# Kernel optimization log

Measured on AMD Instinct MI355X. Metric: run time of the kernel, lower is better.

Reference implementation:

```python
import jax, jax.numpy as jnp
import numpy as np

R, N, E = 3, 50000, 800000
IN, HID, HEADS, OUT = 128, 64, 2, 64


def setup_inputs() -> dict:
    key = jax.random.key(0)
    ks = jax.random.split(key, 12)
    s = 0.05
    return {
        "x": jax.random.normal(ks[0], (N, IN), jnp.float32),
        "src": jax.random.randint(ks[1], (R, E), 0, N, jnp.int32),
        "dst": jax.random.randint(ks[2], (R, E), 0, N, jnp.int32),
        "W1": jax.random.normal(ks[3], (R, IN, HEADS * HID), jnp.float32) * s,
        "al1": jax.random.normal(ks[4], (R, HEADS, HID), jnp.float32) * s,
        "ar1": jax.random.normal(ks[5], (R, HEADS, HID), jnp.float32) * s,
        "b1": jnp.zeros((R, HEADS * HID), jnp.float32),
        "W2": jax.random.normal(ks[6], (R, HEADS * HID, HID), jnp.float32) * s,
        "al2": jax.random.normal(ks[7], (R, 1, HID), jnp.float32) * s,
        "ar2": jax.random.normal(ks[8], (R, 1, HID), jnp.float32) * s,
        "b2": jnp.zeros((R, HID), jnp.float32),
        "Wl": jax.random.normal(ks[9], (HID, OUT), jnp.float32) * s,
        "bl": jnp.zeros((OUT,), jnp.float32),
    }


def gat_conv(x, src, dst, W, al, ar, b, heads, dim):
    """DGL GATConv on a homogeneous edge list: returns elu(aggregated) [N, heads, dim]."""
    n = x.shape[0]
    feat = (x @ W).reshape(n, heads, dim)                     # [N,H,D]
    el = (feat * al).sum(-1)                                  # [N,H]
    er = (feat * ar).sum(-1)                                  # [N,H]
    e = jax.nn.leaky_relu(el[src] + er[dst], 0.2)             # [E,H]
    # segment softmax over incoming edges of each dst node
    m = jax.lax.stop_gradient(jax.ops.segment_max(e, dst, num_segments=n))
    ee = jnp.exp(e - m[dst])                                  # [E,H]
    z = jax.ops.segment_sum(ee, dst, num_segments=n)          # [N,H]
    a = ee / z[dst]                                           # [E,H]
    msg = feat[src] * a[..., None]                            # [E,H,D]
    out = jax.ops.segment_sum(msg, dst, num_segments=n)       # [N,H,D]
    return jax.nn.elu(out + b.reshape(1, heads, dim))


def reference(x, src, dst, W1, al1, ar1, b1, W2, al2, ar2, b2, Wl, bl):
    # layer 1: per-relation GATConv, summed (HeteroGraphConv default aggregate='sum')
    h1 = sum(gat_conv(x, src[r], dst[r], W1[r], al1[r], ar1[r], b1[r], HEADS, HID)
             for r in range(R))                               # [N,H,HID]
    h1 = h1.reshape(N, HEADS * HID)                           # flatten(1)
    # layer 2: single-head GATConv per relation, summed
    h2 = sum(gat_conv(h1, src[r], dst[r], W2[r], al2[r], ar2[r], b2[r], 1, HID)
             for r in range(R))                               # [N,1,HID]
    h2 = h2.mean(1)                                           # mean over the single head
    return h2 @ Wl + bl                                       # [N,OUT]
```

## Files before the change

kernel.cpp:

```cpp
#include <hip/hip_runtime.h>

constexpr int R = 3;
constexpr int N = 50000;
constexpr int E = 800000;
constexpr int K = 128;
constexpr int NT16 = N / 16;
constexpr int GB = (NT16 + 3) / 4;

constexpr int BKT_SH = 9;
constexpr int NBKT = (N + 511) >> 9;
constexpr int BCAP = 10240;
constexpr int P1E = 4096;
constexpr int P1B = (E + P1E - 1) / P1E;

constexpr int NF1 = 192;
constexpr int NF2 = 96;
constexpr int NF3 = 16;

typedef __attribute__((ext_vector_type(8))) short bf16x8;
typedef __attribute__((ext_vector_type(4))) float f32x4;
typedef __attribute__((ext_vector_type(2))) float f32x2;


__device__ inline unsigned short f2bf(float f) {
    unsigned u = __float_as_uint(f);
    u += 0x7FFF + ((u >> 16) & 1);
    return (unsigned short)(u >> 16);
}
__device__ inline float bf2f_lo(unsigned p) { return __uint_as_float(p << 16); }
__device__ inline float bf2f_hi(unsigned p) { return __uint_as_float(p & 0xFFFF0000u); }

__device__ inline float lrelu02(float x) { return fmaxf(x, 0.2f * x); }
__device__ inline float elu1f(float x) { return x > 0.f ? x : __expf(x) - 1.f; }


__global__ __launch_bounds__(256) void bucket_p1(const int* __restrict__ src,
                                                 const int* __restrict__ dst,
                                                 int* __restrict__ gcur,
                                                 uint2* __restrict__ ebuf) {
    __shared__ uint2 img[P1E];
    __shared__ int bins[NBKT], bstart[NBKT], gbase[NBKT];
    __shared__ int sc[128];
    const int r = blockIdx.y;
    const int e0 = blockIdx.x * P1E;
    const int cnt = min(P1E, E - e0);
    const int tid = threadIdx.x;
    if (tid < NBKT) bins[tid] = 0;
    __syncthreads();
    int sv[16], dv[16], rk[16];
    int ni = 0;
    for (int i = tid; i < cnt; i += 256, ni++) {
        sv[ni] = src[(size_t)r * E + e0 + i];
        dv[ni] = dst[(size_t)r * E + e0 + i];
        rk[ni] = atomicAdd(&bins[dv[ni] >> BKT_SH], 1);
    }
    __syncthreads();
    if (tid < 128) sc[tid] = (tid < NBKT) ? bins[tid] : 0;
    __syncthreads();
    for (int off = 1; off < 128; off <<= 1) {
        int v = 0;
        if (tid < 128 && tid >= off) v = sc[tid - off];
        __syncthreads();
        if (tid < 128) sc[tid] += v;
        __syncthreads();
    }
    if (tid < NBKT) bstart[tid] = sc[tid] - bins[tid];
    __syncthreads();
    for (int j = 0; j < ni; j++) {
        int b = dv[j] >> BKT_SH;
        img[bstart[b] + rk[j]] = make_uint2((unsigned)sv[j], (unsigned)dv[j]);
    }
    if (tid < NBKT) gbase[tid] = bins[tid] ? atomicAdd(&gcur[r * NBKT + tid], bins[tid]) : 0;
    __syncthreads();
    for (int i = tid; i < cnt; i += 256) {
        uint2 e = img[i];
        int b = (int)(e.y >> BKT_SH);
        int pos = gbase[b] + (i - bstart[b]);
        if (pos < BCAP) ebuf[(size_t)(r * NBKT + b) * BCAP + pos] = e;
    }
}

__global__ void bucket_scan(const int* __restrict__ gcur, int* __restrict__ bpre) {
    int w = threadIdx.x >> 6, lane = threadIdx.x & 63;
    if (w >= R) return;
    const int* g = gcur + w * NBKT;
    int* p = bpre + w * NBKT;
    int carry = 0;
    for (int base = 0; base < NBKT; base += 64) {
        int v = (base + lane < NBKT) ? g[base + lane] : 0;
        int x = v;
#pragma unroll
        for (int off = 1; off < 64; off <<= 1) {
            int t = __shfl_up(x, off);
            if (lane >= off) x += t;
        }
        if (base + lane < NBKT) p[base + lane] = carry + x - v;
        carry += __shfl(x, 63);
    }
}

__global__ __launch_bounds__(256) void bucket_p2(const uint2* __restrict__ ebuf,
                                                 const int* __restrict__ gcur,
                                                 const int* __restrict__ bpre,
                                                 int* __restrict__ rowptr,
                                                 int* __restrict__ srclist) {
    __shared__ unsigned img[BCAP];
    __shared__ int bins[512], bst[512], cur[512], sc[256];
    const int r = blockIdx.y, b = blockIdx.x;
    const int tid = threadIdx.x;
    const int bcnt = gcur[r * NBKT + b];
    const int gbase = bpre[r * NBKT + b];
    const uint2* reg = ebuf + (size_t)(r * NBKT + b) * BCAP;
    for (int i = tid; i < 512; i += 256) bins[i] = 0;
    __syncthreads();
    for (int i = tid; i < bcnt; i += 256) atomicAdd(&bins[reg[i].y & 511], 1);
    __syncthreads();
    int v0 = bins[2 * tid], v1 = bins[2 * tid + 1];
    sc[tid] = v0 + v1;
    __syncthreads();
    for (int off = 1; off < 256; off <<= 1) {
        int t = 0;
        if (tid >= off) t = sc[tid - off];
        __syncthreads();
        sc[tid] += t;
        __syncthreads();
    }
    int base = sc[tid] - (v0 + v1);
    bst[2 * tid] = base;
    bst[2 * tid + 1] = base + v0;
    cur[2 * tid] = base;
    cur[2 * tid + 1] = base + v0;
    __syncthreads();
    for (int nl = tid; nl < 512; nl += 256) {
        int n = (b << BKT_SH) + nl;
        if (n < N) rowptr[r * (N + 1) + n] = gbase + bst[nl];
    }
    if (b == NBKT - 1 && tid == 0) rowptr[r * (N + 1) + N] = gbase + bcnt;
    for (int i = tid; i < bcnt; i += 256) {
        uint2 e = reg[i];
        int p = atomicAdd(&cur[e.y & 511], 1);
        img[p] = e.x;
    }
    __syncthreads();
    for (int i = tid; i < bcnt; i += 256) srclist[(size_t)r * E + gbase + i] = img[i];
}


__global__ __launch_bounds__(64) void prep_wf(const float* __restrict__ W1,
                                              const float* __restrict__ W2,
                                              const float* __restrict__ Wl,
                                              short* __restrict__ WF1,
                                              short* __restrict__ WF2,
                                              short* __restrict__ WF3) {
    int f = blockIdx.x;
    int lane = threadIdx.x;
    int c = lane & 15, g = lane >> 4;
    const float* srcp;
    int stride;
    short* dstp;
    int hl;
    if (f < NF1) {
        hl = f & 1;
        int h = (f >> 1) & 1, ks = (f >> 2) & 3, tr = (f >> 4) & 3, r = f >> 6;
        int col = h * 64 + tr * 16 + c;
        srcp = W1 + (size_t)r * 128 * 128 + (size_t)(ks * 32 + g * 8) * 128 + col;
        stride = 128;
        dstp = WF1 + (size_t)f * 512 + lane * 8;
    } else if (f < NF1 + NF2) {
        int f2 = f - NF1;
        hl = f2 & 1;
        int ks = (f2 >> 1) & 3, t = f2 >> 3;
        int c192 = t * 16 + c;
        int r = c192 >> 6, col64 = c192 & 63;
        srcp = W2 + (size_t)r * 128 * 64 + (size_t)(ks * 32 + g * 8) * 64 + col64;
        stride = 64;
        dstp = WF2 + (size_t)f2 * 512 + lane * 8;
    } else {
        int f3 = f - NF1 - NF2;
        hl = f3 & 1;
        int ks = (f3 >> 1) & 1, t = f3 >> 2;
        srcp = Wl + (size_t)(ks * 32 + g * 8) * 64 + t * 16 + c;
        stride = 64;
        dstp = WF3 + (size_t)f3 * 512 + lane * 8;
    }
#pragma unroll
    for (int i = 0; i < 8; i++) {
        float v = srcp[(size_t)i * stride];
        unsigned short hi = f2bf(v);
        dstp[i] = hl ? (short)f2bf(v - __uint_as_float(((unsigned)hi) << 16)) : (short)hi;
    }
}


__device__ inline void split_a_p(const float* __restrict__ xrow, bf16x8* ah, bf16x8* al) {
#pragma unroll
    for (int ks = 0; ks < 4; ks++) {
        f32x4 xa = *(const f32x4*)(xrow + ks * 32);
        f32x4 xb = *(const f32x4*)(xrow + ks * 32 + 4);
#pragma unroll
        for (int i = 0; i < 4; i++) {
            unsigned short h = f2bf(xa[i]);
            ah[ks][i] = (short)h;
            al[ks][i] = (short)f2bf(xa[i] - __uint_as_float(((unsigned)h) << 16));
            unsigned short h2 = f2bf(xb[i]);
            ah[ks][4 + i] = (short)h2;
            al[ks][4 + i] = (short)f2bf(xb[i] - __uint_as_float(((unsigned)h2) << 16));
        }
    }
}

__global__ __launch_bounds__(256) void gemm1_mfma(const float* __restrict__ X,
                                                  const short* __restrict__ WF1,
                                                  const float* __restrict__ al1,
                                                  const float* __restrict__ ar1,
                                                  unsigned* __restrict__ packed1,
                                                  float* __restrict__ el,
                                                  float* __restrict__ er) {
    __shared__ float xs[64][132];
    const int n0_blk = blockIdx.x * 64;
    const int tid = threadIdx.x;
    const int rows = min(64, N - n0_blk);
    for (int i = tid; i < rows * 32; i += 256) {
        int row = i >> 5, q4 = i & 31;
        *(f32x4*)&xs[row][q4 * 4] = *(const f32x4*)(X + (size_t)(n0_blk + row) * K + q4 * 4);
    }
    __syncthreads();
    const int lane = tid & 63;
    const int c = lane & 15;
    const int g = lane >> 4;
    const int n0 = n0_blk + (tid >> 6) * 16;
    if (n0 >= N) return;
    bf16x8 ah[4], al[4];
    split_a_p(&xs[(tid >> 6) * 16 + c][g * 8], ah, al);
    const bf16x8* fbase = (const bf16x8*)WF1 + lane;
    for (int r = 0; r < R; r++) {
        float pel0[4] = {0.f, 0.f, 0.f, 0.f}, per0[4] = {0.f, 0.f, 0.f, 0.f};
        float pel1[4] = {0.f, 0.f, 0.f, 0.f}, per1[4] = {0.f, 0.f, 0.f, 0.f};
        for (int tr = 0; tr < 4; tr++) {
            const bf16x8* fb = fbase + (size_t)((r * 4 + tr) * 16) * 64;
            f32x4 acc0 = {0.f, 0.f, 0.f, 0.f};
            f32x4 acc1 = {0.f, 0.f, 0.f, 0.f};
#pragma unroll
            for (int ks = 0; ks < 4; ks++) {
                bf16x8 b0h = fb[(ks * 4 + 0) * 64];
                bf16x8 b0l = fb[(ks * 4 + 1) * 64];
                bf16x8 b1h = fb[(ks * 4 + 2) * 64];
                bf16x8 b1l = fb[(ks * 4 + 3) * 64];
                acc0 = __builtin_amdgcn_mfma_f32_16x16x32_bf16(ah[ks], b0h, acc0, 0, 0, 0);
                acc0 = __builtin_amdgcn_mfma_f32_16x16x32_bf16(al[ks], b0h, acc0, 0, 0, 0);
                acc0 = __builtin_amdgcn_mfma_f32_16x16x32_bf16(ah[ks], b0l, acc0, 0, 0, 0);
                acc1 = __builtin_amdgcn_mfma_f32_16x16x32_bf16(ah[ks], b1h, acc1, 0, 0, 0);
                acc1 = __builtin_amdgcn_mfma_f32_16x16x32_bf16(al[ks], b1h, acc1, 0, 0, 0);
                acc1 = __builtin_amdgcn_mfma_f32_16x16x32_bf16(ah[ks], b1l, acc1, 0, 0, 0);
            }
            float a0 = al1[r * 128 + tr * 16 + c];
            float r0 = ar1[r * 128 + tr * 16 + c];
            float a1 = al1[r * 128 + 64 + tr * 16 + c];
            float r1 = ar1[r * 128 + 64 + tr * 16 + c];
#pragma unroll
            for (int i = 0; i < 4; i++) {
                pel0[i] += acc0[i] * a0;
                per0[i] += acc0[i] * r0;
                pel1[i] += acc1[i] * a1;
                per1[i] += acc1[i] * r1;
                int m = g * 4 + i;
                unsigned wrd = (unsigned)f2bf(acc0[i]) | ((unsigned)f2bf(acc1[i]) << 16);
                packed1[(size_t)(n0 + m) * 192 + r * 64 + tr * 16 + c] = wrd;
            }
        }
#pragma unroll
        for (int off = 1; off < 16; off <<= 1) {
#pragma unroll
            for (int i = 0; i < 4; i++) {
                pel0[i] += __shfl_xor(pel0[i], off);
                per0[i] += __shfl_xor(per0[i], off);
                pel1[i] += __shfl_xor(pel1[i], off);
                per1[i] += __shfl_xor(per1[i], off);
            }
        }
        if (c == 0) {
#pragma unroll
            for (int i = 0; i < 4; i++) {
                int n = n0 + g * 4 + i;
                el[(r * N + n) * 2 + 0] = pel0[i];
                el[(r * N + n) * 2 + 1] = pel1[i];
                er[(r * N + n) * 2 + 0] = per0[i];
                er[(r * N + n) * 2 + 1] = per1[i];
            }
        }
    }
}


__global__ __launch_bounds__(256) void gemm2_mfma(const float* __restrict__ X,
                                                  const short* __restrict__ WF2,
                                                  const float* __restrict__ al2,
                                                  const float* __restrict__ ar2,
                                                  unsigned short* __restrict__ packed2,
                                                  float* __restrict__ el,
                                                  float* __restrict__ er) {
    __shared__ float xs[64][132];
    const int n0_blk = blockIdx.x * 64;
    const int tid = threadIdx.x;
    const int rows = min(64, N - n0_blk);
    for (int i = tid; i < rows * 32; i += 256) {
        int row = i >> 5, q4 = i & 31;
        *(f32x4*)&xs[row][q4 * 4] = *(const f32x4*)(X + (size_t)(n0_blk + row) * K + q4 * 4);
    }
    __syncthreads();
    const int lane = tid & 63;
    const int c = lane & 15;
    const int g = lane >> 4;
    const int n0 = n0_blk + (tid >> 6) * 16;
    if (n0 >= N) return;
    bf16x8 ah[4], al[4];
    split_a_p(&xs[(tid >> 6) * 16 + c][g * 8], ah, al);
    const bf16x8* fbase = (const bf16x8*)WF2 + lane;
    float pel[4], per[4];
    for (int t = 0; t < 12; t++) {
        int r = t >> 2, tt = t & 3;
        if (tt == 0) {
#pragma unroll
            for (int i = 0; i < 4; i++) { pel[i] = 0.f; per[i] = 0.f; }
        }
        f32x4 acc = {0.f, 0.f, 0.f, 0.f};
#pragma unroll
        for (int ks = 0; ks < 4; ks++) {
            bf16x8 vh = fbase[(size_t)((t * 4 + ks) * 2 + 0) * 64];
            bf16x8 vl = fbase[(size_t)((t * 4 + ks) * 2 + 1) * 64];
            acc = __builtin_amdgcn_mfma_f32_16x16x32_bf16(ah[ks], vh, acc, 0, 0, 0);
            acc = __builtin_amdgcn_mfma_f32_16x16x32_bf16(al[ks], vh, acc, 0, 0, 0);
            acc = __builtin_amdgcn_mfma_f32_16x16x32_bf16(ah[ks], vl, acc, 0, 0, 0);
        }
        float a = al2[r * 64 + tt * 16 + c];
        float rr = ar2[r * 64 + tt * 16 + c];
#pragma unroll
        for (int i = 0; i < 4; i++) {
            pel[i] += acc[i] * a;
            per[i] += acc[i] * rr;
            int m = g * 4 + i;
            packed2[(size_t)(n0 + m) * 192 + t * 16 + c] = f2bf(acc[i]);
        }
        if (tt == 3) {
#pragma unroll
            for (int off = 1; off < 16; off <<= 1) {
#pragma unroll
                for (int i = 0; i < 4; i++) {
                    pel[i] += __shfl_xor(pel[i], off);
                    per[i] += __shfl_xor(per[i], off);
                }
            }
            if (c == 0) {
#pragma unroll
                for (int i = 0; i < 4; i++) {
                    int n = n0 + g * 4 + i;
                    el[r * N + n] = pel[i];
                    er[r * N + n] = per[i];
                }
            }
        }
    }
}


__global__ __launch_bounds__(256) void agg_l1(const char* __restrict__ packed1b,
                                              const float* __restrict__ el_,
                                              const float* __restrict__ er_,
                                              const int* __restrict__ rowptr,
                                              const int* __restrict__ srclist,
                                              const float* __restrict__ b1,
                                              float* __restrict__ h1) {
    int n = (blockIdx.x * blockDim.x + threadIdx.x) >> 6;
    int lane = threadIdx.x & 63;
    if (n >= N) return;
    const int q = lane >> 4;
    const int c = lane & 15;
    const unsigned coff = (unsigned)(c * 16);
    const float2* el2 = (const float2*)el_;
    const float2* er2 = (const float2*)er_;
    float hacc0[4] = {0.f, 0.f, 0.f, 0.f}, hacc1[4] = {0.f, 0.f, 0.f, 0.f};
    for (int r = 0; r < R; r++) {
        int beg = rowptr[r * (N + 1) + n];
        int end = rowptr[r * (N + 1) + n + 1];
        float2 ern = er2[r * N + n];
        const int* sl = srclist + r * E;
        const int rbase = r * N;
        const unsigned robf = (unsigned)(r * 256);
        f32x2 acc2[4] = {{0.f, 0.f}, {0.f, 0.f}, {0.f, 0.f}, {0.f, 0.f}};
        float zl0 = 0.f, zl1 = 0.f;
        for (int cbeg = beg; cbeg < end; cbeg += 64) {
            int cnt = min(64, end - cbeg);
            unsigned ofs = 0;
            float ew0 = 0.f, ew1 = 0.f;
            if (lane < cnt) {
                int sid = sl[cbeg + lane];
                float2 e = el2[rbase + sid];
                ew0 = __expf(lrelu02(e.x + ern.x));
                ew1 = __expf(lrelu02(e.y + ern.y));
                ofs = (unsigned)sid * 768u + robf;
            }
            zl0 += ew0;
            zl1 += ew1;
            int kmax = (cnt + 3) & ~3;
            int k = 0;
            for (; k + 8 <= kmax; k += 8) {
                int iA = k + q, iB = k + 4 + q;
                unsigned oA = (unsigned)__shfl((int)ofs, iA);
                unsigned oB = (unsigned)__shfl((int)ofs, iB);
                f32x2 wA = {__shfl(ew0, iA), __shfl(ew1, iA)};
                f32x2 wB = {__shfl(ew0, iB), __shfl(ew1, iB)};
                uint4 vA = *(const uint4*)(packed1b + (oA + coff));
                uint4 vB = *(const uint4*)(packed1b + (oB + coff));
                acc2[0] += (f32x2){bf2f_lo(vA.x), bf2f_hi(vA.x)} * wA;
                acc2[1] += (f32x2){bf2f_lo(vA.y), bf2f_hi(vA.y)} * wA;
                acc2[2] += (f32x2){bf2f_lo(vA.z), bf2f_hi(vA.z)} * wA;
                acc2[3] += (f32x2){bf2f_lo(vA.w), bf2f_hi(vA.w)} * wA;
                acc2[0] += (f32x2){bf2f_lo(vB.x), bf2f_hi(vB.x)} * wB;
                acc2[1] += (f32x2){bf2f_lo(vB.y), bf2f_hi(vB.y)} * wB;
                acc2[2] += (f32x2){bf2f_lo(vB.z), bf2f_hi(vB.z)} * wB;
                acc2[3] += (f32x2){bf2f_lo(vB.w), bf2f_hi(vB.w)} * wB;
            }
            if (k < kmax) {
                int idx = k + q;
                unsigned o = (unsigned)__shfl((int)ofs, idx);
                f32x2 w = {__shfl(ew0, idx), __shfl(ew1, idx)};
                uint4 v = *(const uint4*)(packed1b + (o + coff));
                acc2[0] += (f32x2){bf2f_lo(v.x), bf2f_hi(v.x)} * w;
                acc2[1] += (f32x2){bf2f_lo(v.y), bf2f_hi(v.y)} * w;
                acc2[2] += (f32x2){bf2f_lo(v.z), bf2f_hi(v.z)} * w;
                acc2[3] += (f32x2){bf2f_lo(v.w), bf2f_hi(v.w)} * w;
            }
        }
#pragma unroll
        for (int i = 0; i < 4; i++) {
            acc2[i].x += __shfl_xor(acc2[i].x, 16);
            acc2[i].x += __shfl_xor(acc2[i].x, 32);
            acc2[i].y += __shfl_xor(acc2[i].y, 16);
            acc2[i].y += __shfl_xor(acc2[i].y, 32);
        }
#pragma unroll
        for (int off = 32; off; off >>= 1) {
            zl0 += __shfl_xor(zl0, off);
            zl1 += __shfl_xor(zl1, off);
        }
        float rz0 = (end > beg) ? __builtin_amdgcn_rcpf(zl0) : 0.f;
        float rz1 = (end > beg) ? __builtin_amdgcn_rcpf(zl1) : 0.f;
        float4 bv0 = *(const float4*)(b1 + r * 128 + c * 4);
        float4 bv1 = *(const float4*)(b1 + r * 128 + 64 + c * 4);
        hacc0[0] += elu1f(acc2[0].x * rz0 + bv0.x);
        hacc0[1] += elu1f(acc2[1].x * rz0 + bv0.y);
        hacc0[2] += elu1f(acc2[2].x * rz0 + bv0.z);
        hacc0[3] += elu1f(acc2[3].x * rz0 + bv0.w);
        hacc1[0] += elu1f(acc2[0].y * rz1 + bv1.x);
        hacc1[1] += elu1f(acc2[1].y * rz1 + bv1.y);
        hacc1[2] += elu1f(acc2[2].y * rz1 + bv1.z);
        hacc1[3] += elu1f(acc2[3].y * rz1 + bv1.w);
    }
    if (q == 0) {
        float4 o0 = {hacc0[0], hacc0[1], hacc0[2], hacc0[3]};
        float4 o1 = {hacc1[0], hacc1[1], hacc1[2], hacc1[3]};
        *(float4*)(h1 + (size_t)n * 128 + c * 4) = o0;
        *(float4*)(h1 + (size_t)n * 128 + 64 + c * 4) = o1;
    }
}

__global__ __launch_bounds__(256) void agg_l2(const char* __restrict__ packed2b,
                                              const float* __restrict__ el,
                                              const float* __restrict__ er,
                                              const int* __restrict__ rowptr,
                                              const int* __restrict__ srclist,
                                              const float* __restrict__ b2,
                                              float* __restrict__ h2) {
    int n = (blockIdx.x * blockDim.x + threadIdx.x) >> 6;
    int lane = threadIdx.x & 63;
    if (n >= N) return;
    const int q = lane >> 4;
    const int c = lane & 15;
    const unsigned coff = (unsigned)(c * 8);
    float hacc[4] = {0.f, 0.f, 0.f, 0.f};
    for (int r = 0; r < R; r++) {
        int beg = rowptr[r * (N + 1) + n];
        int end = rowptr[r * (N + 1) + n + 1];
        float ern = er[r * N + n];
        const int* sl = srclist + r * E;
        const int rbase = r * N;
        const unsigned robf = (unsigned)(r * 128);
        f32x2 acc01 = {0.f, 0.f}, acc23 = {0.f, 0.f};
        float zl = 0.f;
        for (int cbeg = beg; cbeg < end; cbeg += 64) {
            int cnt = min(64, end - cbeg);
            unsigned ofs = 0;
            float ew = 0.f;
            if (lane < cnt) {
                int sid = sl[cbeg + lane];
                ew = __expf(lrelu02(el[rbase + sid] + ern));
                ofs = (unsigned)sid * 384u + robf;
            }
            zl += ew;
            int kmax = (cnt + 3) & ~3;
            int k = 0;
            for (; k + 8 <= kmax; k += 8) {
                int iA = k + q, iB = k + 4 + q;
                unsigned oA = (unsigned)__shfl((int)ofs, iA);
                unsigned oB = (unsigned)__shfl((int)ofs, iB);
                float aA = __shfl(ew, iA), aB = __shfl(ew, iB);
                uint2 vA = *(const uint2*)(packed2b + (oA + coff));
                uint2 vB = *(const uint2*)(packed2b + (oB + coff));
                f32x2 wA = {aA, aA}, wB = {aB, aB};
                acc01 += (f32x2){bf2f_lo(vA.x), bf2f_hi(vA.x)} * wA;
                acc23 += (f32x2){bf2f_lo(vA.y), bf2f_hi(vA.y)} * wA;
                acc01 += (f32x2){bf2f_lo(vB.x), bf2f_hi(vB.x)} * wB;
                acc23 += (f32x2){bf2f_lo(vB.y), bf2f_hi(vB.y)} * wB;
            }
            if (k < kmax) {
                int idx = k + q;
                unsigned o = (unsigned)__shfl((int)ofs, idx);
                float a = __shfl(ew, idx);
                uint2 v = *(const uint2*)(packed2b + (o + coff));
                f32x2 w = {a, a};
                acc01 += (f32x2){bf2f_lo(v.x), bf2f_hi(v.x)} * w;
                acc23 += (f32x2){bf2f_lo(v.y), bf2f_hi(v.y)} * w;
            }
        }
        acc01.x += __shfl_xor(acc01.x, 16); acc01.x += __shfl_xor(acc01.x, 32);
        acc01.y += __shfl_xor(acc01.y, 16); acc01.y += __shfl_xor(acc01.y, 32);
        acc23.x += __shfl_xor(acc23.x, 16); acc23.x += __shfl_xor(acc23.x, 32);
        acc23.y += __shfl_xor(acc23.y, 16); acc23.y += __shfl_xor(acc23.y, 32);
#pragma unroll
        for (int off = 32; off; off >>= 1) zl += __shfl_xor(zl, off);
        float rz = (end > beg) ? __builtin_amdgcn_rcpf(zl) : 0.f;
        float4 bv = *(const float4*)(b2 + r * 64 + c * 4);
        hacc[0] += elu1f(acc01.x * rz + bv.x);
        hacc[1] += elu1f(acc01.y * rz + bv.y);
        hacc[2] += elu1f(acc23.x * rz + bv.z);
        hacc[3] += elu1f(acc23.y * rz + bv.w);
    }
    if (q == 0) {
        float4 o = {hacc[0], hacc[1], hacc[2], hacc[3]};
        *(float4*)(h2 + (size_t)n * 64 + c * 4) = o;
    }
}


__global__ __launch_bounds__(256) void gemm3_mfma(const float* __restrict__ h2,
                                                  const short* __restrict__ WF3,
                                                  const float* __restrict__ bl,
                                                  float* __restrict__ out) {
    __shared__ float xs[64][68];
    const int n0_blk = blockIdx.x * 64;
    const int tid = threadIdx.x;
    const int rows = min(64, N - n0_blk);
    for (int i = tid; i < rows * 16; i += 256) {
        int row = i >> 4, q4 = i & 15;
        *(f32x4*)&xs[row][q4 * 4] = *(const f32x4*)(h2 + (size_t)(n0_blk + row) * 64 + q4 * 4);
    }
    __syncthreads();
    const int lane = tid & 63;
    const int c = lane & 15;
    const int g = lane >> 4;
    const int n0 = n0_blk + (tid >> 6) * 16;
    if (n0 >= N) return;
    bf16x8 ah[2], al[2];
    const float* xrow = &xs[(tid >> 6) * 16 + c][g * 8];
#pragma unroll
    for (int ks = 0; ks < 2; ks++) {
        f32x4 xa = *(const f32x4*)(xrow + ks * 32);
        f32x4 xb = *(const f32x4*)(xrow + ks * 32 + 4);
#pragma unroll
        for (int i = 0; i < 4; i++) {
            unsigned short h = f2bf(xa[i]);
            ah[ks][i] = (short)h;
            al[ks][i] = (short)f2bf(xa[i] - __uint_as_float(((unsigned)h) << 16));
            unsigned short h2v = f2bf(xb[i]);
            ah[ks][4 + i] = (short)h2v;
            al[ks][4 + i] = (short)f2bf(xb[i] - __uint_as_float(((unsigned)h2v) << 16));
        }
    }
    const bf16x8* fbase = (const bf16x8*)WF3 + lane;
    for (int t = 0; t < 4; t++) {
        f32x4 acc = {0.f, 0.f, 0.f, 0.f};
#pragma unroll
        for (int ks = 0; ks < 2; ks++) {
            bf16x8 vh = fbase[((t * 2 + ks) * 2 + 0) * 64];
            bf16x8 vl = fbase[((t * 2 + ks) * 2 + 1) * 64];
            acc = __builtin_amdgcn_mfma_f32_16x16x32_bf16(ah[ks], vh, acc, 0, 0, 0);
            acc = __builtin_amdgcn_mfma_f32_16x16x32_bf16(al[ks], vh, acc, 0, 0, 0);
            acc = __builtin_amdgcn_mfma_f32_16x16x32_bf16(ah[ks], vl, acc, 0, 0, 0);
        }
        float bb = bl[t * 16 + c];
#pragma unroll
        for (int i = 0; i < 4; i++) {
            out[(size_t)(n0 + g * 4 + i) * 64 + t * 16 + c] = acc[i] + bb;
        }
    }
}


extern "C" void kernel_launch(void* const* d_in, const int* in_sizes, int n_in,
                              void* d_out, int out_size, void* d_ws, size_t ws_size,
                              hipStream_t stream) {
    const float* x   = (const float*)d_in[0];
    const int*   src = (const int*)d_in[1];
    const int*   dst = (const int*)d_in[2];
    const float* W1  = (const float*)d_in[3];
    const float* al1 = (const float*)d_in[4];
    const float* ar1 = (const float*)d_in[5];
    const float* b1  = (const float*)d_in[6];
    const float* W2  = (const float*)d_in[7];
    const float* al2 = (const float*)d_in[8];
    const float* ar2 = (const float*)d_in[9];
    const float* b2  = (const float*)d_in[10];
    const float* Wl  = (const float*)d_in[11];
    const float* bl  = (const float*)d_in[12];
    float* out = (float*)d_out;

    char* ws = (char*)d_ws;
    size_t off = 0;
    auto alloc = [&](size_t bytes) {
        char* p = ws + off;
        off += (bytes + 255) & ~(size_t)255;
        return p;
    };
    unsigned*       packed1 = (unsigned*)alloc(sizeof(unsigned) * (size_t)N * R * 64);
    unsigned short* packed2 = (unsigned short*)alloc(sizeof(unsigned short) * (size_t)N * R * 64);
    float* h1      = (float*)alloc(sizeof(float) * (size_t)N * 128);
    float* h2      = (float*)alloc(sizeof(float) * (size_t)N * 64);
    float* el1     = (float*)alloc(sizeof(float) * (size_t)R * N * 2);
    float* er1     = (float*)alloc(sizeof(float) * (size_t)R * N * 2);
    float* el2     = (float*)alloc(sizeof(float) * (size_t)R * N);
    float* er2     = (float*)alloc(sizeof(float) * (size_t)R * N);
    int*   rowptr  = (int*)alloc(sizeof(int) * (size_t)R * (N + 1));
    int*   srclist = (int*)alloc(sizeof(int) * (size_t)R * E);
    uint2* ebuf    = (uint2*)alloc(sizeof(uint2) * (size_t)R * NBKT * BCAP);
    int*   gcur    = (int*)alloc(sizeof(int) * (size_t)R * NBKT);
    int*   bpre    = (int*)alloc(sizeof(int) * (size_t)R * NBKT);
    short* WF1     = (short*)alloc(sizeof(short) * (size_t)NF1 * 512);
    short* WF2     = (short*)alloc(sizeof(short) * (size_t)NF2 * 512);
    short* WF3     = (short*)alloc(sizeof(short) * (size_t)NF3 * 512);

    hipMemsetAsync(gcur, 0, sizeof(int) * (size_t)R * NBKT, stream);
    prep_wf<<<NF1 + NF2 + NF3, 64, 0, stream>>>(W1, W2, Wl, WF1, WF2, WF3);
    {
        dim3 g1(P1B, R);
        bucket_p1<<<g1, 256, 0, stream>>>(src, dst, gcur, ebuf);
        bucket_scan<<<1, 192, 0, stream>>>(gcur, bpre);
        dim3 g2(NBKT, R);
        bucket_p2<<<g2, 256, 0, stream>>>(ebuf, gcur, bpre, rowptr, srclist);
    }

    gemm1_mfma<<<GB, 256, 0, stream>>>(x, WF1, al1, ar1, packed1, el1, er1);
    agg_l1<<<(N * 64 + 255) / 256, 256, 0, stream>>>((const char*)packed1, el1, er1,
                                                     rowptr, srclist, b1, h1);

    gemm2_mfma<<<GB, 256, 0, stream>>>(h1, WF2, al2, ar2, packed2, el2, er2);
    agg_l2<<<(N * 64 + 255) / 256, 256, 0, stream>>>((const char*)packed2, el2, er2,
                                                     rowptr, srclist, b2, h2);

    gemm3_mfma<<<GB, 256, 0, stream>>>(h2, WF3, bl, out);
}
```

Measured before the change: 281.2 us.

## Fuse graph bucketing, weight prep and layer-1 GEMM into two launches

Merges prep_wf with bucket pass 1 into one kernel using block-index partitioning. It also merges bucket pass 2 with gemm1 into a second kernel, so independent work runs concurrently. The separate bucket_scan kernel is removed: each pass-2 block computes its own prefix by summing gcur over earlier buckets with a wavefront reduction. This cuts launch count and serialization between small kernels. In exchange, the merged kernels share a larger shared-memory footprint, which may lower occupancy, and the prefix sums are computed redundantly per block.

```diff
diff --git a/kernel.cpp b/kernel.cpp
--- a/kernel.cpp
+++ b/kernel.cpp
@@ -16,6 +16,7 @@
 constexpr int NF1 = 192;
 constexpr int NF2 = 96;
 constexpr int NF3 = 16;
+constexpr int PREP_BLKS = (NF1 + NF2 + NF3) / 4;
 
 typedef __attribute__((ext_vector_type(8))) short bf16x8;
 typedef __attribute__((ext_vector_type(4))) float f32x4;
@@ -34,126 +35,11 @@
 __device__ inline float elu1f(float x) { return x > 0.f ? x : __expf(x) - 1.f; }
 
 
-__global__ __launch_bounds__(256) void bucket_p1(const int* __restrict__ src,
-                                                 const int* __restrict__ dst,
-                                                 int* __restrict__ gcur,
-                                                 uint2* __restrict__ ebuf) {
-    __shared__ uint2 img[P1E];
-    __shared__ int bins[NBKT], bstart[NBKT], gbase[NBKT];
-    __shared__ int sc[128];
-    const int r = blockIdx.y;
-    const int e0 = blockIdx.x * P1E;
-    const int cnt = min(P1E, E - e0);
-    const int tid = threadIdx.x;
-    if (tid < NBKT) bins[tid] = 0;
-    __syncthreads();
-    int sv[16], dv[16], rk[16];
-    int ni = 0;
-    for (int i = tid; i < cnt; i += 256, ni++) {
-        sv[ni] = src[(size_t)r * E + e0 + i];
-        dv[ni] = dst[(size_t)r * E + e0 + i];
-        rk[ni] = atomicAdd(&bins[dv[ni] >> BKT_SH], 1);
-    }
-    __syncthreads();
-    if (tid < 128) sc[tid] = (tid < NBKT) ? bins[tid] : 0;
-    __syncthreads();
-    for (int off = 1; off < 128; off <<= 1) {
-        int v = 0;
-        if (tid < 128 && tid >= off) v = sc[tid - off];
-        __syncthreads();
-        if (tid < 128) sc[tid] += v;
-        __syncthreads();
-    }
-    if (tid < NBKT) bstart[tid] = sc[tid] - bins[tid];
-    __syncthreads();
-    for (int j = 0; j < ni; j++) {
-        int b = dv[j] >> BKT_SH;
-        img[bstart[b] + rk[j]] = make_uint2((unsigned)sv[j], (unsigned)dv[j]);
-    }
-    if (tid < NBKT) gbase[tid] = bins[tid] ? atomicAdd(&gcur[r * NBKT + tid], bins[tid]) : 0;
-    __syncthreads();
-    for (int i = tid; i < cnt; i += 256) {
-        uint2 e = img[i];
-        int b = (int)(e.y >> BKT_SH);
-        int pos = gbase[b] + (i - bstart[b]);
-        if (pos < BCAP) ebuf[(size_t)(r * NBKT + b) * BCAP + pos] = e;
-    }
-}
-
-__global__ void bucket_scan(const int* __restrict__ gcur, int* __restrict__ bpre) {
-    int w = threadIdx.x >> 6, lane = threadIdx.x & 63;
-    if (w >= R) return;
-    const int* g = gcur + w * NBKT;
-    int* p = bpre + w * NBKT;
-    int carry = 0;
-    for (int base = 0; base < NBKT; base += 64) {
-        int v = (base + lane < NBKT) ? g[base + lane] : 0;
-        int x = v;
-#pragma unroll
-        for (int off = 1; off < 64; off <<= 1) {
-            int t = __shfl_up(x, off);
-            if (lane >= off) x += t;
-        }
-        if (base + lane < NBKT) p[base + lane] = carry + x - v;
-        carry += __shfl(x, 63);
-    }
-}
-
-__global__ __launch_bounds__(256) void bucket_p2(const uint2* __restrict__ ebuf,
-                                                 const int* __restrict__ gcur,
-                                                 const int* __restrict__ bpre,
-                                                 int* __restrict__ rowptr,
-                                                 int* __restrict__ srclist) {
-    __shared__ unsigned img[BCAP];
-    __shared__ int bins[512], bst[512], cur[512], sc[256];
-    const int r = blockIdx.y, b = blockIdx.x;
-    const int tid = threadIdx.x;
-    const int bcnt = gcur[r * NBKT + b];
-    const int gbase = bpre[r * NBKT + b];
-    const uint2* reg = ebuf + (size_t)(r * NBKT + b) * BCAP;
-    for (int i = tid; i < 512; i += 256) bins[i] = 0;
-    __syncthreads();
-    for (int i = tid; i < bcnt; i += 256) atomicAdd(&bins[reg[i].y & 511], 1);
-    __syncthreads();
-    int v0 = bins[2 * tid], v1 = bins[2 * tid + 1];
-    sc[tid] = v0 + v1;
-    __syncthreads();
-    for (int off = 1; off < 256; off <<= 1) {
-        int t = 0;
-        if (tid >= off) t = sc[tid - off];
-        __syncthreads();
-        sc[tid] += t;
-        __syncthreads();
-    }
-    int base = sc[tid] - (v0 + v1);
-    bst[2 * tid] = base;
-    bst[2 * tid + 1] = base + v0;
-    cur[2 * tid] = base;
-    cur[2 * tid + 1] = base + v0;
-    __syncthreads();
-    for (int nl = tid; nl < 512; nl += 256) {
-        int n = (b << BKT_SH) + nl;
-        if (n < N) rowptr[r * (N + 1) + n] = gbase + bst[nl];
-    }
-    if (b == NBKT - 1 && tid == 0) rowptr[r * (N + 1) + N] = gbase + bcnt;
-    for (int i = tid; i < bcnt; i += 256) {
-        uint2 e = reg[i];
-        int p = atomicAdd(&cur[e.y & 511], 1);
-        img[p] = e.x;
-    }
-    __syncthreads();
-    for (int i = tid; i < bcnt; i += 256) srclist[(size_t)r * E + gbase + i] = img[i];
-}
-
-
-__global__ __launch_bounds__(64) void prep_wf(const float* __restrict__ W1,
-                                              const float* __restrict__ W2,
-                                              const float* __restrict__ Wl,
-                                              short* __restrict__ WF1,
-                                              short* __restrict__ WF2,
-                                              short* __restrict__ WF3) {
-    int f = blockIdx.x;
-    int lane = threadIdx.x;
+__device__ void prep_frag(int f, int lane,
+                          const float* __restrict__ W1, const float* __restrict__ W2,
+                          const float* __restrict__ Wl,
+                          short* __restrict__ WF1, short* __restrict__ WF2,
+                          short* __restrict__ WF3) {
     int c = lane & 15, g = lane >> 4;
     const float* srcp;
     int stride;
@@ -191,6 +77,64 @@
     }
 }
 
+__global__ __launch_bounds__(256) void fusedA(const int* __restrict__ src,
+                                              const int* __restrict__ dst,
+                                              int* __restrict__ gcur,
+                                              uint2* __restrict__ ebuf,
+                                              const float* __restrict__ W1,
+                                              const float* __restrict__ W2,
+                                              const float* __restrict__ Wl,
+                                              short* __restrict__ WF1,
+                                              short* __restrict__ WF2,
+                                              short* __restrict__ WF3) {
+    __shared__ uint2 img[P1E];
+    __shared__ int bins[NBKT], bstart[NBKT], gbase[NBKT];
+    __shared__ int sc[128];
+    const int tid = threadIdx.x;
+    if (blockIdx.x < PREP_BLKS) {
+        int f = blockIdx.x * 4 + (tid >> 6);
+        prep_frag(f, tid & 63, W1, W2, Wl, WF1, WF2, WF3);
+        return;
+    }
+    const int pbid = blockIdx.x - PREP_BLKS;
+    const int r = pbid / P1B;
+    const int e0 = (pbid % P1B) * P1E;
+    const int cnt = min(P1E, E - e0);
+    if (tid < NBKT) bins[tid] = 0;
+    __syncthreads();
+    int sv[16], dv[16], rk[16];
+    int ni = 0;
+    for (int i = tid; i < cnt; i += 256, ni++) {
+        sv[ni] = src[(size_t)r * E + e0 + i];
+        dv[ni] = dst[(size_t)r * E + e0 + i];
+        rk[ni] = atomicAdd(&bins[dv[ni] >> BKT_SH], 1);
+    }
+    __syncthreads();
+    if (tid < 128) sc[tid] = (tid < NBKT) ? bins[tid] : 0;
+    __syncthreads();
+    for (int off = 1; off < 128; off <<= 1) {
+        int v = 0;
+        if (tid < 128 && tid >= off) v = sc[tid - off];
+        __syncthreads();
+        if (tid < 128) sc[tid] += v;
+        __syncthreads();
+    }
+    if (tid < NBKT) bstart[tid] = sc[tid] - bins[tid];
+    __syncthreads();
+    for (int j = 0; j < ni; j++) {
+        int b = dv[j] >> BKT_SH;
+        img[bstart[b] + rk[j]] = make_uint2((unsigned)sv[j], (unsigned)dv[j]);
+    }
+    if (tid < NBKT) gbase[tid] = bins[tid] ? atomicAdd(&gcur[r * NBKT + tid], bins[tid]) : 0;
+    __syncthreads();
+    for (int i = tid; i < cnt; i += 256) {
+        uint2 e = img[i];
+        int b = (int)(e.y >> BKT_SH);
+        int pos = gbase[b] + (i - bstart[b]);
+        if (pos < BCAP) ebuf[(size_t)(r * NBKT + b) * BCAP + pos] = e;
+    }
+}
+
 
 __device__ inline void split_a_p(const float* __restrict__ xrow, bf16x8* ah, bf16x8* al) {
 #pragma unroll
@@ -209,16 +153,77 @@
     }
 }
 
-__global__ __launch_bounds__(256) void gemm1_mfma(const float* __restrict__ X,
-                                                  const short* __restrict__ WF1,
-                                                  const float* __restrict__ al1,
-                                                  const float* __restrict__ ar1,
-                                                  unsigned* __restrict__ packed1,
-                                                  float* __restrict__ el,
-                                                  float* __restrict__ er) {
-    __shared__ float xs[64][132];
-    const int n0_blk = blockIdx.x * 64;
+__global__ __launch_bounds__(256) void fusedB(const uint2* __restrict__ ebuf,
+                                              const int* __restrict__ gcur,
+                                              int* __restrict__ rowptr,
+                                              int* __restrict__ srclist,
+                                              const float* __restrict__ X,
+                                              const short* __restrict__ WF1,
+                                              const float* __restrict__ al1,
+                                              const float* __restrict__ ar1,
+                                              unsigned* __restrict__ packed1,
+                                              float* __restrict__ el,
+                                              float* __restrict__ er) {
+    alignas(16) __shared__ char smB[48128];
+    __shared__ int gbase_s;
     const int tid = threadIdx.x;
+    if (blockIdx.x < R * NBKT) {
+        unsigned* img = (unsigned*)smB;
+        int* bins = (int*)(smB + BCAP * 4);
+        int* bst = bins + 512;
+        int* cur = bst + 512;
+        int* sc = cur + 512;
+        const int r = blockIdx.x / NBKT, b = blockIdx.x % NBKT;
+        const int bcnt = gcur[r * NBKT + b];
+        const uint2* reg = ebuf + (size_t)(r * NBKT + b) * BCAP;
+        for (int i = tid; i < 512; i += 256) bins[i] = 0;
+        if (tid < 64) {
+            int acc = 0;
+            for (int base = 0; base < NBKT; base += 64) {
+                int idx = base + tid;
+                int v = (idx < b) ? gcur[r * NBKT + idx] : 0;
+#pragma unroll
+                for (int off = 32; off; off >>= 1) v += __shfl_xor(v, off);
+                acc += v;
+            }
+            if (tid == 0) gbase_s = acc;
+        }
+        __syncthreads();
+        const int gbase = gbase_s;
+        for (int i = tid; i < bcnt; i += 256) atomicAdd(&bins[reg[i].y & 511], 1);
+        __syncthreads();
+        int v0 = bins[2 * tid], v1 = bins[2 * tid + 1];
+        sc[tid] = v0 + v1;
+        __syncthreads();
+        for (int off = 1; off < 256; off <<= 1) {
+            int t = 0;
+            if (tid >= off) t = sc[tid - off];
+            __syncthreads();
+            sc[tid] += t;
+            __syncthreads();
+        }
+        int base = sc[tid] - (v0 + v1);
+        bst[2 * tid] = base;
+        bst[2 * tid + 1] = base + v0;
+        cur[2 * tid] = base;
+        cur[2 * tid + 1] = base + v0;
+        __syncthreads();
+        for (int nl = tid; nl < 512; nl += 256) {
+            int n = (b << BKT_SH) + nl;
+            if (n < N) rowptr[r * (N + 1) + n] = gbase + bst[nl];
+        }
+        if (b == NBKT - 1 && tid == 0) rowptr[r * (N + 1) + N] = gbase + bcnt;
+        for (int i = tid; i < bcnt; i += 256) {
+            uint2 e = reg[i];
+            int p = atomicAdd(&cur[e.y & 511], 1);
+            img[p] = e.x;
+        }
+        __syncthreads();
+        for (int i = tid; i < bcnt; i += 256) srclist[(size_t)r * E + gbase + i] = img[i];
+        return;
+    }
+    float (*xs)[132] = (float(*)[132])smB;
+    const int n0_blk = (blockIdx.x - R * NBKT) * 64;
     const int rows = min(64, N - n0_blk);
     for (int i = tid; i < rows * 32; i += 256) {
         int row = i >> 5, q4 = i & 31;
@@ -633,22 +638,18 @@
     int*   srclist = (int*)alloc(sizeof(int) * (size_t)R * E);
     uint2* ebuf    = (uint2*)alloc(sizeof(uint2) * (size_t)R * NBKT * BCAP);
     int*   gcur    = (int*)alloc(sizeof(int) * (size_t)R * NBKT);
-    int*   bpre    = (int*)alloc(sizeof(int) * (size_t)R * NBKT);
     short* WF1     = (short*)alloc(sizeof(short) * (size_t)NF1 * 512);
     short* WF2     = (short*)alloc(sizeof(short) * (size_t)NF2 * 512);
     short* WF3     = (short*)alloc(sizeof(short) * (size_t)NF3 * 512);
 
     hipMemsetAsync(gcur, 0, sizeof(int) * (size_t)R * NBKT, stream);
-    prep_wf<<<NF1 + NF2 + NF3, 64, 0, stream>>>(W1, W2, Wl, WF1, WF2, WF3);
-    {
-        dim3 g1(P1B, R);
-        bucket_p1<<<g1, 256, 0, stream>>>(src, dst, gcur, ebuf);
-        bucket_scan<<<1, 192, 0, stream>>>(gcur, bpre);
-        dim3 g2(NBKT, R);
-        bucket_p2<<<g2, 256, 0, stream>>>(ebuf, gcur, bpre, rowptr, srclist);
-    }
-
-    gemm1_mfma<<<GB, 256, 0, stream>>>(x, WF1, al1, ar1, packed1, el1, er1);
+
+    fusedA<<<PREP_BLKS + R * P1B, 256, 0, stream>>>(src, dst, gcur, ebuf,
+                                                    W1, W2, Wl, WF1, WF2, WF3);
+
+    fusedB<<<R * NBKT + GB, 256, 0, stream>>>(ebuf, gcur, rowptr, srclist,
+                                              x, WF1, al1, ar1, packed1, el1, er1);
+
     agg_l1<<<(N * 64 + 255) / 256, 256, 0, stream>>>((const char*)packed1, el1, er1,
                                                      rowptr, srclist, b1, h1);
 
```

Result: no change. 277.5 us (-1.3%).
